# Kernel optimization log

Hardware: AMD Instinct MI355X
Metric: run time of the kernel (lower is better)

The kernel has to match this reference:

```python
import jax, jax.numpy as jnp
import numpy as np

K = 1024      # codebook_size
D = 64        # embedding_dim
DECAY = 0.99
EPS = 1e-05


def setup_inputs() -> dict:
    key = jax.random.key(0)
    k1, k2, k3 = jax.random.split(key, 3)
    z_e = jax.random.normal(k1, (16, D, 64, 64), dtype=jnp.float32)
    emb = jax.random.normal(k2, (D, K), dtype=jnp.float32) * 0.05
    emb_ema = emb  # buffer initialized as clone of emb
    counts_ema = jnp.zeros((K,), dtype=jnp.float32)
    return {"z_e": z_e, "emb": emb, "emb_ema": emb_ema, "counts_ema": counts_ema}


def reference(z_e, emb, emb_ema, counts_ema):
    B, Dd, H, W = z_e.shape
    # [B,D,H,W] -> [B*H*W, D]
    z = jnp.transpose(z_e, (0, 2, 3, 1)).reshape(-1, Dd)
    # squared L2 distance to each code: [N, K]
    dist = (z * z).sum(1, keepdims=True) - 2.0 * (z @ emb) + (emb * emb).sum(0, keepdims=True)
    idx = jnp.argmin(dist, axis=1)                      # [N]
    embeddings = emb.T[idx]                             # [N, D]
    z_q = z + jax.lax.stop_gradient(embeddings - z)     # straight-through

    # EMA codebook update (no_grad in original)
    zg = jax.lax.stop_gradient(z)
    counts = jnp.zeros((K,), dtype=emb.dtype).at[idx].add(1.0)          # one-hot column sums
    counts_ema_new = counts_ema + (1.0 - DECAY) * (counts - counts_ema)
    emb_update = jax.ops.segment_sum(zg, idx, num_segments=K).T          # [D, K]
    emb_ema_new = emb_ema + (1.0 - DECAY) * (emb_update - emb_ema)
    n = counts_ema_new.sum()
    counts_norm = (counts_ema_new + EPS) / (n + K * EPS) * n
    emb_new = emb_ema_new / counts_norm[None, :]

    z_q_out = jnp.transpose(z_q.reshape(B, H, W, Dd), (0, 3, 1, 2))      # back to [B,D,H,W]
    idx_out = idx.reshape(B, H, W)
    return z_q_out, idx_out, emb_new, emb_ema_new, counts_ema_new
```

## Files before the change

### kernel.cpp

```cpp
#include <hip/hip_runtime.h>
#include <math.h>

#define KCODES 1024
#define DDIM   64
#define NCOPY  4

constexpr size_t O_ZQ  = 0;
constexpr size_t O_IDX = 4194304;
constexpr size_t O_EMB = O_IDX + 65536;
constexpr size_t O_EMA = O_EMB + 65536;
constexpr size_t O_CEN = O_EMA + 65536;

constexpr size_t W_UPD   = 0;
constexpr size_t W_CNT   = 262144;
constexpr size_t W_ENORM = 266240;
constexpr size_t W_EN2   = 267264;
constexpr size_t W_EMAXA = 268288;
constexpr size_t W_FLAGN = 268304;
constexpr size_t W_FLAGL = 268320;
constexpr int    FLAGCAP = 8192;
constexpr size_t W_EMBT  = 276512;
constexpr size_t W_G16H  = 342048;
constexpr size_t W_G16L  = 374816;

typedef _Float16 f16;
typedef f16 f16x8 __attribute__((ext_vector_type(8)));
typedef float f32x4 __attribute__((ext_vector_type(4)));

#define MF(a, b, c) __builtin_amdgcn_mfma_f32_16x16x32_f16((a), (b), (c), 0, 0, 0)

static __device__ __forceinline__ void gload16(const void* g, void* l) {
  __builtin_amdgcn_global_load_lds(
      (const __attribute__((address_space(1))) void*)g,
      (__attribute__((address_space(3))) void*)l, 16, 0, 0);
}

__global__ __launch_bounds__(256) void vq_prep(const float* __restrict__ emb,
                                               float* __restrict__ ws) {
  __shared__ float t_lds[64 * 65];
  const int tid = threadIdx.x;
  const int g   = blockIdx.x;

  if (g < 16) {
    const int k0 = g * 64;
    #pragma unroll
    for (int it = 0; it < 16; ++it) {
      const int idx = tid + it * 256;
      const int d   = idx >> 6;
      const int kq  = idx & 63;
      t_lds[d * 65 + kq] = emb[d * KCODES + k0 + kq];
    }
    __syncthreads();

    f16* gh = (f16*)(ws + W_G16H);
    f16* gl = (f16*)(ws + W_G16L);
    #pragma unroll
    for (int it = 0; it < 16; ++it) {
      const int idx = tid + it * 256;
      const int kk  = idx >> 6;
      const int d   = idx & 63;
      const float v = t_lds[d * 65 + kk];
      ws[W_EMBT + (size_t)(k0 + kk) * 64 + d] = v;
      const f16 hi = (f16)v;
      const f16 lo = (f16)(v - (float)hi);
      const int u  = (d >> 3) ^ (kk & 7);
      const size_t fo = (size_t)g * 4096 + kk * 64 + u * 8 + (d & 7);
      gh[fo] = hi;
      gl[fo] = lo;
    }

    if (tid < 64) {
      const int k = tid;
      float s = 0.f;
      #pragma unroll
      for (int d = 0; d < DDIM; ++d) {
        const float v = t_lds[d * 65 + k];
        s = fmaf(v, v, s);
      }
      ws[W_ENORM + k0 + k] = s;
      ws[W_EN2   + k0 + k] = -0.5f * s;
      float mx = s;
      #pragma unroll
      for (int off = 1; off < 64; off <<= 1) mx = fmaxf(mx, __shfl_xor(mx, off, 64));
      if (tid == 0) ws[W_EMAXA + g] = mx;
    }
  }

  {
    float4* base = (float4*)(ws + W_UPD);
    const int total4 = 66560;
    for (int idx = g * 256 + tid; idx < total4; idx += 64 * 256)
      base[idx] = float4{0.f, 0.f, 0.f, 0.f};
  }
  if (g == 0 && tid == 0) ((int*)(ws + W_FLAGN))[0] = 0;
}

#define ZP 132
__global__ __launch_bounds__(256, 3) void vq_main(
    const float* __restrict__ z_e,
    const float* __restrict__ g16h,
    const float* __restrict__ g16l,
    const float* __restrict__ embT,
    const float* __restrict__ en2,
    const float* __restrict__ emaxa,
    float* __restrict__ upd,
    float* __restrict__ cnt,
    int*   __restrict__ flagn,
    int*   __restrict__ flagl,
    float* __restrict__ out) {
  __shared__ float z_lds[DDIM * ZP];
  __shared__ __align__(16) f16 e_hi[2][2048];
  __shared__ __align__(16) f16 e_lo[2][2048];
  __shared__ int bidx[128];

  const int tid  = threadIdx.x;
  const int bid  = blockIdx.x;
  const int wv   = tid >> 6;
  const int lane = tid & 63;
  const int m    = lane & 15;
  const int q    = lane >> 4;
  const int r0   = wv * 32 + m;
  const int r1   = r0 + 16;

  float* updc = upd + ((size_t)(bid & (NCOPY - 1)) << 16);
  float* cntc = cnt + ((size_t)(bid & (NCOPY - 1)) << 10);

  const int n0  = bid * 128;
  const int b   = n0 >> 12;
  const int hw0 = n0 & 4095;
  const size_t zbase = (size_t)b * 262144 + (size_t)hw0;

  {
    gload16((const char*)g16h + tid * 16, (char*)&e_hi[0][0] + tid * 16);
    gload16((const char*)g16l + tid * 16, (char*)&e_lo[0][0] + tid * 16);
  }

  {
    const float4* z4 = (const float4*)(z_e + zbase);
    #pragma unroll
    for (int it = 0; it < 8; ++it) {
      const int f  = tid + it * 256;
      const int d  = f >> 5;
      const int r4 = f & 31;
      const float4 v = z4[(size_t)d * 1024 + r4];
      *(float4*)(z_lds + d * ZP + r4 * 4) = v;
    }
  }

  float emax = 0.f;
  {
    const float4* e4 = (const float4*)emaxa;
    #pragma unroll
    for (int i = 0; i < 4; ++i) {
      const float4 v = e4[i];
      emax = fmaxf(emax, fmaxf(fmaxf(v.x, v.y), fmaxf(v.z, v.w)));
    }
  }
  __syncthreads();

  f16x8 b0h_0, b1h_0, b0l_0, b1l_0, b0h_1, b1h_1, b0l_1, b1l_1;
  float zz0 = 0.f, zz1 = 0.f;
  #pragma unroll
  for (int j = 0; j < 8; ++j) {
    const int d0 = q * 8 + j, d1 = 32 + q * 8 + j;
    const float v00 = z_lds[d0 * ZP + r0];
    const float v01 = z_lds[d1 * ZP + r0];
    const float v10 = z_lds[d0 * ZP + r1];
    const float v11 = z_lds[d1 * ZP + r1];
    zz0 = fmaf(v00, v00, zz0); zz0 = fmaf(v01, v01, zz0);
    zz1 = fmaf(v10, v10, zz1); zz1 = fmaf(v11, v11, zz1);
    const f16 h00 = (f16)v00, h01 = (f16)v01, h10 = (f16)v10, h11 = (f16)v11;
    b0h_0[j] = h00; b1h_0[j] = h01; b0h_1[j] = h10; b1h_1[j] = h11;
    b0l_0[j] = (f16)(v00 - (float)h00);
    b1l_0[j] = (f16)(v01 - (float)h01);
    b0l_1[j] = (f16)(v10 - (float)h10);
    b1l_1[j] = (f16)(v11 - (float)h11);
  }
  zz0 += __shfl_xor(zz0, 16, 64); zz0 += __shfl_xor(zz0, 32, 64);
  zz1 += __shfl_xor(zz1, 16, 64); zz1 += __shfl_xor(zz1, 32, 64);

  const int lcl7  = m & 7;
  const int aoff0 = m * 128 + ((q)     ^ lcl7) * 16;
  const int aoff1 = m * 128 + ((4 + q) ^ lcl7) * 16;

  float M1_0 = -INFINITY, M2_0 = -INFINITY, M1_1 = -INFINITY, M2_1 = -INFINITY;
  int   I1_0 = 0, I1_1 = 0;

  #pragma unroll 1
  for (int c = 0; c < 32; ++c) {
    const int cb = c & 1;
    if (c < 31) {
      const int nb = cb ^ 1;
      const size_t so = (size_t)(c + 1) * 4096 + tid * 16;
      gload16((const char*)g16h + so, (char*)&e_hi[nb][0] + tid * 16);
      gload16((const char*)g16l + so, (char*)&e_lo[nb][0] + tid * 16);
    }
    const char* eb = (const char*)&e_hi[cb][0];
    const char* lb = (const char*)&e_lo[cb][0];
    __builtin_amdgcn_s_setprio(1);
    #pragma unroll
    for (int t = 0; t < 2; ++t) {
      const f16x8 a0h = *(const f16x8*)(eb + t * 2048 + aoff0);
      const f16x8 a1h = *(const f16x8*)(eb + t * 2048 + aoff1);
      const f16x8 a0l = *(const f16x8*)(lb + t * 2048 + aoff0);
      const f16x8 a1l = *(const f16x8*)(lb + t * 2048 + aoff1);
      const f32x4 en2f = *(const f32x4*)(en2 + c * 32 + t * 16 + q * 4);
      f32x4 acc0 = en2f, acc1 = en2f;
      acc0 = MF(a0l, b0h_0, acc0);  acc1 = MF(a0l, b0h_1, acc1);
      acc0 = MF(a1l, b1h_0, acc0);  acc1 = MF(a1l, b1h_1, acc1);
      acc0 = MF(a0h, b0l_0, acc0);  acc1 = MF(a0h, b0l_1, acc1);
      acc0 = MF(a1h, b1l_0, acc0);  acc1 = MF(a1h, b1l_1, acc1);
      acc0 = MF(a0h, b0h_0, acc0);  acc1 = MF(a0h, b0h_1, acc1);
      acc0 = MF(a1h, b1h_0, acc0);  acc1 = MF(a1h, b1h_1, acc1);
      const int ib = c * 32 + t * 16 + q * 4;
      #pragma unroll
      for (int r = 0; r < 4; ++r) {
        const float a = acc0[r];
        const bool gt = a > M1_0;
        M2_0 = fmaxf(M2_0, fminf(a, M1_0));
        if (gt) I1_0 = ib + r;
        M1_0 = fmaxf(M1_0, a);
        const float a1v = acc1[r];
        const bool gt1 = a1v > M1_1;
        M2_1 = fmaxf(M2_1, fminf(a1v, M1_1));
        if (gt1) I1_1 = ib + r;
        M1_1 = fmaxf(M1_1, a1v);
      }
    }
    __builtin_amdgcn_s_setprio(0);
    __syncthreads();
  }

  #pragma unroll
  for (int off = 16; off <= 32; off <<= 1) {
    {
      const float o1 = __shfl_xor(M1_0, off, 64);
      const float o2 = __shfl_xor(M2_0, off, 64);
      const int   oi = __shfl_xor(I1_0, off, 64);
      const float nm2 = fmaxf(fmaxf(M2_0, o2), fminf(M1_0, o1));
      if (o1 > M1_0) I1_0 = oi;
      M1_0 = fmaxf(M1_0, o1);
      M2_0 = nm2;
    }
    {
      const float o1 = __shfl_xor(M1_1, off, 64);
      const float o2 = __shfl_xor(M2_1, off, 64);
      const int   oi = __shfl_xor(I1_1, off, 64);
      const float nm2 = fmaxf(fmaxf(M2_1, o2), fminf(M1_1, o1));
      if (o1 > M1_1) I1_1 = oi;
      M1_1 = fmaxf(M1_1, o1);
      M2_1 = nm2;
    }
  }

  if (lane < 32) {
    const int s   = lane >> 4;
    const int row = wv * 32 + s * 16 + m;
    const float MM1 = s ? M1_1 : M1_0;
    const float MM2 = s ? M2_1 : M2_0;
    const int   II  = s ? I1_1 : I1_0;
    const float zzv = s ? zz1 : zz0;
    const float Mh = 5.0e-5f * sqrtf(zzv * emax);
    if (MM1 - MM2 > Mh) {
      bidx[row] = II;
      out[O_IDX + n0 + row] = (float)II;
      atomicAdd(cntc + II, 1.0f);
    } else {
      bidx[row] = -1;
      const int sl = atomicAdd(flagn, 1);
      if (sl < FLAGCAP) flagl[sl] = n0 + row;
    }
  }
  __syncthreads();

  {
    const int row  = tid & 127;
    const int half = tid >> 7;
    const int code = bidx[row];
    if (code >= 0) {
      const float4* er4 = (const float4*)(embT + (size_t)code * 64);
      #pragma unroll
      for (int qq = 0; qq < 8; ++qq) {
        const float4 e4 = er4[half * 8 + qq];
        const float ev[4] = {e4.x, e4.y, e4.z, e4.w};
        #pragma unroll
        for (int x = 0; x < 4; ++x) {
          const int d = half * 32 + qq * 4 + x;
          const float zv = z_lds[d * ZP + row];
          out[O_ZQ + zbase + (size_t)d * 4096 + row] = zv + (ev[x] - zv);
        }
      }
    }
  }

  {
    #pragma unroll 4
    for (int rr = 0; rr < 32; ++rr) {
      const int row  = wv * 32 + rr;
      const int code = bidx[row];
      if (code >= 0)
        atomicAdd(updc + (size_t)code * 64 + lane, z_lds[lane * ZP + row]);
    }
  }
}

__global__ __launch_bounds__(256) void vq_rescore(
    const float* __restrict__ z_e,
    const float* __restrict__ embT,
    const float* __restrict__ eN,
    const int* __restrict__ flagn,
    const int* __restrict__ flagl,
    float* __restrict__ upd,
    float* __restrict__ cnt,
    float* __restrict__ out) {
  __shared__ float zrow[64];
  __shared__ float wv_v[4];
  __shared__ int   wv_i[4];
  __shared__ int   bestc;

  const int tid = threadIdx.x;
  int nf = *flagn;
  if (nf > FLAGCAP) nf = FLAGCAP;

  for (int j = blockIdx.x; j < nf; j += gridDim.x) {
    __syncthreads();
    const int rowid = flagl[j];
    const int bb = rowid >> 12;
    const int hw = rowid & 4095;
    const size_t base = (size_t)bb * 262144 + (size_t)hw;
    if (tid < 64) zrow[tid] = z_e[base + (size_t)tid * 4096];
    __syncthreads();

    float bm = INFINITY;
    int   bi = 0;
    #pragma unroll
    for (int cc = 0; cc < 4; ++cc) {
      const int k = tid * 4 + cc;
      const float4* e4p = (const float4*)(embT + (size_t)k * 64);
      float a0 = 0.f, a1 = 0.f, a2 = 0.f, a3 = 0.f;
      #pragma unroll
      for (int d4 = 0; d4 < 16; ++d4) {
        const float4 e4 = e4p[d4];
        a0 = fmaf(zrow[d4 * 4 + 0], e4.x, a0);
        a1 = fmaf(zrow[d4 * 4 + 1], e4.y, a1);
        a2 = fmaf(zrow[d4 * 4 + 2], e4.z, a2);
        a3 = fmaf(zrow[d4 * 4 + 3], e4.w, a3);
      }
      const float dist = fmaf(-2.f, (a0 + a1) + (a2 + a3), eN[k]);
      if (dist < bm) { bm = dist; bi = k; }
    }
    #pragma unroll
    for (int mm = 1; mm < 64; mm <<= 1) {
      const float v2 = __shfl_xor(bm, mm, 64);
      const int   i2 = __shfl_xor(bi, mm, 64);
      if (v2 < bm || (v2 == bm && i2 < bi)) { bm = v2; bi = i2; }
    }
    if ((tid & 63) == 0) { wv_v[tid >> 6] = bm; wv_i[tid >> 6] = bi; }
    __syncthreads();
    if (tid == 0) {
      float v = wv_v[0]; int ix = wv_i[0];
      #pragma unroll
      for (int w = 1; w < 4; ++w) {
        if (wv_v[w] < v || (wv_v[w] == v && wv_i[w] < ix)) { v = wv_v[w]; ix = wv_i[w]; }
      }
      bestc = ix;
      out[O_IDX + rowid] = (float)ix;
      atomicAdd(cnt + ix, 1.0f);
    }
    __syncthreads();
    if (tid < 64) {
      const int d = tid;
      const float zv = zrow[d];
      const float ev = embT[(size_t)bestc * 64 + d];
      out[O_ZQ + base + (size_t)d * 4096] = zv + (ev - zv);
      atomicAdd(upd + (size_t)bestc * 64 + d, zv);
    }
  }
}

__global__ __launch_bounds__(256) void vq_final(const float* __restrict__ emb_ema,
                                                const float* __restrict__ counts_ema,
                                                const float* __restrict__ ws,
                                                float* __restrict__ out) {
  __shared__ float red[256];
  const int tid = threadIdx.x;
  const float* cnt = ws + W_CNT;
  const float* upd = ws + W_UPD;

  float psum = 0.f;
  for (int t = tid; t < KCODES; t += 256) {
    float c = 0.f;
    #pragma unroll
    for (int p = 0; p < NCOPY; ++p) c += cnt[p * KCODES + t];
    const float ce  = counts_ema[t];
    const float cen = ce + 0.01f * (c - ce);
    psum += cen;
    if (blockIdx.x == 0) out[O_CEN + t] = cen;
  }
  red[tid] = psum;
  __syncthreads();
  #pragma unroll
  for (int s = 128; s > 0; s >>= 1) {
    if (tid < s) red[tid] += red[tid + s];
    __syncthreads();
  }
  const float nsum = red[0];

  const int i = blockIdx.x * 256 + tid;
  const int d = i >> 10;
  const int k = i & 1023;

  float c = 0.f;
  #pragma unroll
  for (int p = 0; p < NCOPY; ++p) c += cnt[p * KCODES + k];
  const float ce  = counts_ema[k];
  const float cen = ce + 0.01f * (c - ce);
  const float norm = (cen + 1e-5f) / (nsum + (float)KCODES * 1e-5f) * nsum;

  float us = 0.f;
  #pragma unroll
  for (int p = 0; p < NCOPY; ++p) us += upd[(size_t)p * 65536 + (size_t)k * 64 + d];
  const float ema     = emb_ema[i];
  const float ema_new = ema + 0.01f * (us - ema);
  out[O_EMA + i] = ema_new;
  out[O_EMB + i] = ema_new / norm;
}

extern "C" void kernel_launch(void* const* d_in, const int* in_sizes, int n_in,
                              void* d_out, int out_size, void* d_ws, size_t ws_size,
                              hipStream_t stream) {
  const float* z_e        = (const float*)d_in[0];
  const float* emb        = (const float*)d_in[1];
  const float* emb_ema    = (const float*)d_in[2];
  const float* counts_ema = (const float*)d_in[3];
  float* out = (float*)d_out;
  float* ws  = (float*)d_ws;

  vq_prep<<<64, 256, 0, stream>>>(emb, ws);
  vq_main<<<512, 256, 0, stream>>>(z_e, ws + W_G16H, ws + W_G16L,
                                   ws + W_EMBT, ws + W_EN2, ws + W_EMAXA,
                                   ws + W_UPD, ws + W_CNT,
                                   (int*)(ws + W_FLAGN), (int*)(ws + W_FLAGL), out);
  vq_rescore<<<256, 256, 0, stream>>>(z_e, ws + W_EMBT, ws + W_ENORM,
                                      (int*)(ws + W_FLAGN), (int*)(ws + W_FLAGL),
                                      ws + W_UPD, ws + W_CNT, out);
  vq_final<<<256, 256, 0, stream>>>(emb_ema, counts_ema, ws, out);
}
```

Baseline: 152.7 us.

## Give each wave a private double-buffered codebook stream, removing block barriers

Each wave now streams its own copy of the fp16 hi/lo codebook chunks into a private double-buffered LDS region and uses vmcnt/lgkmcnt waits in place of a block-wide __syncthreads per chunk. Chunks are 16 codes over 64 iterations, and the code norms are staged in LDS instead of being read from global memory. This removes barrier stalls between waves. In exchange, each wave issues its own loads (four times the codebook traffic per block) and uses more LDS, so launch bounds drop to two blocks per CU. The loop also issues extra wrap-around prefetches on the last two iterations that are never consumed.

```diff
diff --git a/kernel.cpp b/kernel.cpp
--- a/kernel.cpp
+++ b/kernel.cpp
@@ -96,7 +96,7 @@
 }
 
 #define ZP 132
-__global__ __launch_bounds__(256, 3) void vq_main(
+__global__ __launch_bounds__(256, 2) void vq_main(
     const float* __restrict__ z_e,
     const float* __restrict__ g16h,
     const float* __restrict__ g16l,
@@ -109,8 +109,8 @@
     int*   __restrict__ flagl,
     float* __restrict__ out) {
   __shared__ float z_lds[DDIM * ZP];
-  __shared__ __align__(16) f16 e_hi[2][2048];
-  __shared__ __align__(16) f16 e_lo[2][2048];
+  __shared__ __align__(16) f16 e_buf[16384];
+  __shared__ __align__(16) float en2_lds[KCODES];
   __shared__ int bidx[128];
 
   const int tid  = threadIdx.x;
@@ -130,9 +130,21 @@
   const int hw0 = n0 & 4095;
   const size_t zbase = (size_t)b * 262144 + (size_t)hw0;
 
-  {
-    gload16((const char*)g16h + tid * 16, (char*)&e_hi[0][0] + tid * 16);
-    gload16((const char*)g16l + tid * 16, (char*)&e_lo[0][0] + tid * 16);
+  char* ebase = (char*)e_buf + wv * 8192;
+  const char* gh = (const char*)g16h;
+  const char* gl = (const char*)g16l;
+
+  {
+    const size_t go0 = (size_t)lane * 16;
+    gload16(gh + go0,        ebase);
+    gload16(gh + go0 + 1024, ebase + 1024);
+    gload16(gl + go0,        ebase + 2048);
+    gload16(gl + go0 + 1024, ebase + 3072);
+    const size_t go1 = 2048 + (size_t)lane * 16;
+    gload16(gh + go1,        ebase + 4096);
+    gload16(gh + go1 + 1024, ebase + 5120);
+    gload16(gl + go1,        ebase + 6144);
+    gload16(gl + go1 + 1024, ebase + 7168);
   }
 
   {
@@ -146,6 +158,7 @@
       *(float4*)(z_lds + d * ZP + r4 * 4) = v;
     }
   }
+  ((float4*)en2_lds)[tid] = ((const float4*)en2)[tid];
 
   float emax = 0.f;
   {
@@ -187,48 +200,49 @@
   int   I1_0 = 0, I1_1 = 0;
 
   #pragma unroll 1
-  for (int c = 0; c < 32; ++c) {
-    const int cb = c & 1;
-    if (c < 31) {
-      const int nb = cb ^ 1;
-      const size_t so = (size_t)(c + 1) * 4096 + tid * 16;
-      gload16((const char*)g16h + so, (char*)&e_hi[nb][0] + tid * 16);
-      gload16((const char*)g16l + so, (char*)&e_lo[nb][0] + tid * 16);
-    }
-    const char* eb = (const char*)&e_hi[cb][0];
-    const char* lb = (const char*)&e_lo[cb][0];
+  for (int c = 0; c < 64; ++c) {
+    const int s = c & 1;
+    asm volatile("s_waitcnt vmcnt(4)" ::: "memory");
     __builtin_amdgcn_s_setprio(1);
-    #pragma unroll
-    for (int t = 0; t < 2; ++t) {
-      const f16x8 a0h = *(const f16x8*)(eb + t * 2048 + aoff0);
-      const f16x8 a1h = *(const f16x8*)(eb + t * 2048 + aoff1);
-      const f16x8 a0l = *(const f16x8*)(lb + t * 2048 + aoff0);
-      const f16x8 a1l = *(const f16x8*)(lb + t * 2048 + aoff1);
-      const f32x4 en2f = *(const f32x4*)(en2 + c * 32 + t * 16 + q * 4);
-      f32x4 acc0 = en2f, acc1 = en2f;
-      acc0 = MF(a0l, b0h_0, acc0);  acc1 = MF(a0l, b0h_1, acc1);
-      acc0 = MF(a1l, b1h_0, acc0);  acc1 = MF(a1l, b1h_1, acc1);
-      acc0 = MF(a0h, b0l_0, acc0);  acc1 = MF(a0h, b0l_1, acc1);
-      acc0 = MF(a1h, b1l_0, acc0);  acc1 = MF(a1h, b1l_1, acc1);
-      acc0 = MF(a0h, b0h_0, acc0);  acc1 = MF(a0h, b0h_1, acc1);
-      acc0 = MF(a1h, b1h_0, acc0);  acc1 = MF(a1h, b1h_1, acc1);
-      const int ib = c * 32 + t * 16 + q * 4;
-      #pragma unroll
-      for (int r = 0; r < 4; ++r) {
-        const float a = acc0[r];
-        const bool gt = a > M1_0;
-        M2_0 = fmaxf(M2_0, fminf(a, M1_0));
-        if (gt) I1_0 = ib + r;
-        M1_0 = fmaxf(M1_0, a);
-        const float a1v = acc1[r];
-        const bool gt1 = a1v > M1_1;
-        M2_1 = fmaxf(M2_1, fminf(a1v, M1_1));
-        if (gt1) I1_1 = ib + r;
-        M1_1 = fmaxf(M1_1, a1v);
-      }
+    const char* hb = ebase + s * 4096;
+    const char* lb = hb + 2048;
+    const f16x8 a0h = *(const f16x8*)(hb + aoff0);
+    const f16x8 a1h = *(const f16x8*)(hb + aoff1);
+    const f16x8 a0l = *(const f16x8*)(lb + aoff0);
+    const f16x8 a1l = *(const f16x8*)(lb + aoff1);
+    const f32x4 en2f = *(const f32x4*)(en2_lds + c * 16 + q * 4);
+    f32x4 acc0 = en2f, acc1 = en2f;
+    acc0 = MF(a0l, b0h_0, acc0);  acc1 = MF(a0l, b0h_1, acc1);
+    acc0 = MF(a1l, b1h_0, acc0);  acc1 = MF(a1l, b1h_1, acc1);
+    acc0 = MF(a0h, b0l_0, acc0);  acc1 = MF(a0h, b0l_1, acc1);
+    acc0 = MF(a1h, b1l_0, acc0);  acc1 = MF(a1h, b1l_1, acc1);
+    acc0 = MF(a0h, b0h_0, acc0);  acc1 = MF(a0h, b0h_1, acc1);
+    acc0 = MF(a1h, b1h_0, acc0);  acc1 = MF(a1h, b1h_1, acc1);
+    const int ib = c * 16 + q * 4;
+    #pragma unroll
+    for (int r = 0; r < 4; ++r) {
+      const float a = acc0[r];
+      const bool gt = a > M1_0;
+      M2_0 = fmaxf(M2_0, fminf(a, M1_0));
+      if (gt) I1_0 = ib + r;
+      M1_0 = fmaxf(M1_0, a);
+      const float a1v = acc1[r];
+      const bool gt1 = a1v > M1_1;
+      M2_1 = fmaxf(M2_1, fminf(a1v, M1_1));
+      if (gt1) I1_1 = ib + r;
+      M1_1 = fmaxf(M1_1, a1v);
     }
     __builtin_amdgcn_s_setprio(0);
-    __syncthreads();
+    asm volatile("s_waitcnt lgkmcnt(0)" ::: "memory");
+    {
+      const int cn = (c + 2) & 63;
+      const size_t go = (size_t)cn * 2048 + (size_t)lane * 16;
+      char* dst = ebase + s * 4096;
+      gload16(gh + go,        dst);
+      gload16(gh + go + 1024, dst + 1024);
+      gload16(gl + go,        dst + 2048);
+      gload16(gl + go + 1024, dst + 3072);
+    }
   }
 
   #pragma unroll
```

Result: no change. 154.5 us (+1.2%).
